# Performance work log

Measured on AMD Instinct MI355X. Metric: run time of the kernel, lower is better.

## Reference

```python
import jax, jax.numpy as jnp
import numpy as np

N = 20000      # nodes
E = 320000     # edges
D = 512        # width
L = 4          # layers
VOCAB = 256
MAX_POS = 256
EPS = 1e-5


def setup_inputs() -> dict:
    key = jax.random.key(0)
    ks = jax.random.split(key, 12)
    tokens = jax.random.randint(ks[0], (N,), 0, VOCAB)
    pos = jax.random.randint(ks[1], (N,), 0, MAX_POS)
    edge_index = jax.random.randint(ks[2], (2, E), 0, N)
    vocab_emb = jax.random.normal(ks[3], (VOCAB, D), jnp.float32) * 0.05
    pos_emb = jax.random.normal(ks[4], (MAX_POS, D), jnp.float32) * 0.05
    bn_gamma = jnp.ones((L, D), jnp.float32)
    bn_beta = jnp.zeros((L, D), jnp.float32)
    bn_mean = jax.random.normal(ks[5], (L, D), jnp.float32) * 0.1
    bn_var = jax.random.uniform(ks[6], (L, D), jnp.float32, 0.5, 1.5)
    W_rel = jax.random.normal(ks[7], (L, D, D), jnp.float32) * (1.0 / np.sqrt(D))
    b_rel = jnp.zeros((L, D), jnp.float32)
    W_root = jax.random.normal(ks[8], (L, D, D), jnp.float32) * (1.0 / np.sqrt(D))
    return {
        "tokens": tokens, "pos": pos, "edge_index": edge_index,
        "vocab_emb": vocab_emb, "pos_emb": pos_emb,
        "bn_gamma": bn_gamma, "bn_beta": bn_beta,
        "bn_mean": bn_mean, "bn_var": bn_var,
        "W_rel": W_rel, "b_rel": b_rel, "W_root": W_root,
    }


def reference(tokens, pos, edge_index, vocab_emb, pos_emb,
              bn_gamma, bn_beta, bn_mean, bn_var, W_rel, b_rel, W_root):
    src, dst = edge_index[0], edge_index[1]
    # in-degree for mean aggregation (clamped to 1 like PyG mean aggr)
    deg = jax.ops.segment_sum(jnp.ones((E,), jnp.float32), dst, num_segments=N)
    deg = jnp.maximum(deg, 1.0)[:, None]                     # [N,1]

    x = vocab_emb[tokens] + pos_emb[pos]                     # [N,D]
    for l in range(L):
        # BatchNorm1d, eval mode with running stats
        inv = bn_gamma[l] * jax.lax.rsqrt(bn_var[l] + EPS)
        x = (x - bn_mean[l]) * inv + bn_beta[l]
        # GraphConv: W_root x_i + W_rel * mean_{j->i} x_j + b
        agg = jax.ops.segment_sum(x[src], dst, num_segments=N) / deg
        x = agg @ W_rel[l].T + b_rel[l] + x @ W_root[l].T
        x = jax.nn.relu(x)
    return x
```

## Files before the change

### kernel.cpp

```cpp
#include <hip/hip_runtime.h>
#include <cstdint>

#define EPS 1e-5f

typedef __attribute__((ext_vector_type(8))) short bf16x8;
typedef __attribute__((ext_vector_type(4))) float f32x4;

__device__ __forceinline__ unsigned short f2bf(float x) {
    uint32_t u = __float_as_uint(x);
    u += 0x7fffu + ((u >> 16) & 1u);
    return (unsigned short)(u >> 16);
}
__device__ __forceinline__ uint32_t pack2(float lo, float hi) {
    return (uint32_t)f2bf(lo) | ((uint32_t)f2bf(hi) << 16);
}
__device__ __forceinline__ float bflo(uint32_t p) { return __uint_as_float(p << 16); }
__device__ __forceinline__ float bfhi(uint32_t p) { return __uint_as_float(p & 0xffff0000u); }

__device__ __forceinline__ void async_ld16(const void* g, const void* l) {
    __builtin_amdgcn_global_load_lds(
        (const __attribute__((address_space(1))) uint32_t*)(uintptr_t)g,
        (__attribute__((address_space(3))) uint32_t*)(uint32_t)(uintptr_t)l,
        16, 0, 0);
}

__global__ __launch_bounds__(256) void zero_kernel(int* __restrict__ p, int n) {
    int i = blockIdx.x * 256 + threadIdx.x;
    if (i < n) p[i] = 0;
}

__global__ __launch_bounds__(256) void count_kernel(const int* __restrict__ ei,
                                                    int* __restrict__ deg, int E) {
    int e = blockIdx.x * 256 + threadIdx.x;
    if (e < E) atomicAdd(&deg[ei[E + e]], 1);
}

__global__ __launch_bounds__(1024) void scan_kernel(const int* __restrict__ deg,
                                                    int* __restrict__ offsets,
                                                    int* __restrict__ cursor,
                                                    float* __restrict__ deginv, int N) {
    __shared__ int part[1024];
    const int t = threadIdx.x;
    const int CH = (N + 1023) >> 10;
    const int base = t * CH;
    int s = 0;
    for (int j = 0; j < CH; ++j) {
        int idx = base + j;
        if (idx < N) s += deg[idx];
    }
    part[t] = s;
    __syncthreads();
    for (int off = 1; off < 1024; off <<= 1) {
        int add = (t >= off) ? part[t - off] : 0;
        __syncthreads();
        part[t] += add;
        __syncthreads();
    }
    int run = (t == 0) ? 0 : part[t - 1];
    for (int j = 0; j < CH; ++j) {
        int idx = base + j;
        if (idx < N) {
            offsets[idx] = run;
            cursor[idx]  = run;
            int dgi = deg[idx];
            deginv[idx] = 1.0f / (float)(dgi > 0 ? dgi : 1);
            run += dgi;
        }
    }
    if (t == 1023) offsets[N] = run;
}

__global__ __launch_bounds__(256) void fill_kernel(const int* __restrict__ ei,
                                                   int* __restrict__ cursor,
                                                   int* __restrict__ csr, int E) {
    int e = blockIdx.x * 256 + threadIdx.x;
    if (e < E) {
        int dd = ei[E + e];
        int slot = atomicAdd(&cursor[dd], 1);
        csr[slot] = ei[e];
    }
}

__global__ __launch_bounds__(256) void embed_bn_kernel(const int* __restrict__ tok,
                                                       const int* __restrict__ pos,
                                                       const float* __restrict__ vemb,
                                                       const float* __restrict__ pemb,
                                                       const float* __restrict__ gamma,
                                                       const float* __restrict__ beta,
                                                       const float* __restrict__ mean,
                                                       const float* __restrict__ var,
                                                       uint32_t* __restrict__ Acat, int N) {
    const int idx = blockIdx.x * 256 + threadIdx.x;
    if (idx >= N * 128) return;
    const int row = idx >> 7;
    const int c = (idx & 127) * 4;
    const int tk = tok[row];
    const int ps = pos[row];
    const float4 a = *(const float4*)&vemb[(size_t)tk * 512 + c];
    const float4 b = *(const float4*)&pemb[(size_t)ps * 512 + c];
    const float4 g = *(const float4*)&gamma[c];
    const float4 be = *(const float4*)&beta[c];
    const float4 mn = *(const float4*)&mean[c];
    const float4 vr = *(const float4*)&var[c];
    const float y0 = (a.x + b.x - mn.x) * (g.x * rsqrtf(vr.x + EPS)) + be.x;
    const float y1 = (a.y + b.y - mn.y) * (g.y * rsqrtf(vr.y + EPS)) + be.y;
    const float y2 = (a.z + b.z - mn.z) * (g.z * rsqrtf(vr.z + EPS)) + be.z;
    const float y3 = (a.w + b.w - mn.w) * (g.w * rsqrtf(vr.w + EPS)) + be.w;
    uint2 o;
    o.x = pack2(y0, y1);
    o.y = pack2(y2, y3);
    *(uint2*)&Acat[(size_t)row * 512 + (c >> 1)] = o;
}

__global__ __launch_bounds__(256) void castW_kernel(const float* __restrict__ Wroot,
                                                    const float* __restrict__ Wrel,
                                                    uint32_t* __restrict__ Wcat) {
    const int p = blockIdx.x * 256 + threadIdx.x;
    const int o  = p >> 9;
    const int dp = p & 511;
    float2 v;
    if (dp < 256) v = *(const float2*)&Wroot[(size_t)o * 512 + dp * 2];
    else          v = *(const float2*)&Wrel[(size_t)o * 512 + (dp - 256) * 2];
    Wcat[(size_t)o * 512 + dp] = pack2(v.x, v.y);
}

__global__ __launch_bounds__(256) void castW4_kernel(const float* __restrict__ Wroot,
                                                     const float* __restrict__ Wrel,
                                                     uint32_t* __restrict__ Wcat4) {
    const int p = blockIdx.x * 256 + threadIdx.x;
    const int l   = p >> 18;
    const int rem = p & 262143;
    const int o   = rem >> 9;
    const int dp  = rem & 511;
    float2 v;
    if (dp < 256) v = *(const float2*)&Wroot[(size_t)l * 262144 + (size_t)o * 512 + dp * 2];
    else          v = *(const float2*)&Wrel[(size_t)l * 262144 + (size_t)o * 512 + (dp - 256) * 2];
    Wcat4[(size_t)l * 262144 + (size_t)o * 512 + dp] = pack2(v.x, v.y);
}

__global__ __launch_bounds__(256) void aggregate_kernel(uint32_t* __restrict__ Acat,
                                                        const int* __restrict__ offsets,
                                                        const int* __restrict__ csr,
                                                        const float* __restrict__ deginv,
                                                        int N) {
    const int node = blockIdx.x * 4 + (threadIdx.x >> 6);
    if (node >= N) return;
    const int lane = threadIdx.x & 63;
    const int col = lane * 4;
    const int beg = offsets[node];
    const int end = offsets[node + 1];
    float s[8] = {0.f, 0.f, 0.f, 0.f, 0.f, 0.f, 0.f, 0.f};
    int e = beg;
    for (; e + 4 <= end; e += 4) {
        const int i0 = csr[e];
        const int i1 = csr[e + 1];
        const int i2 = csr[e + 2];
        const int i3 = csr[e + 3];
        const uint4 p0 = *(const uint4*)&Acat[(size_t)i0 * 512 + col];
        const uint4 p1 = *(const uint4*)&Acat[(size_t)i1 * 512 + col];
        const uint4 p2 = *(const uint4*)&Acat[(size_t)i2 * 512 + col];
        const uint4 p3 = *(const uint4*)&Acat[(size_t)i3 * 512 + col];
        s[0] += bflo(p0.x) + bflo(p1.x) + bflo(p2.x) + bflo(p3.x);
        s[1] += bfhi(p0.x) + bfhi(p1.x) + bfhi(p2.x) + bfhi(p3.x);
        s[2] += bflo(p0.y) + bflo(p1.y) + bflo(p2.y) + bflo(p3.y);
        s[3] += bfhi(p0.y) + bfhi(p1.y) + bfhi(p2.y) + bfhi(p3.y);
        s[4] += bflo(p0.z) + bflo(p1.z) + bflo(p2.z) + bflo(p3.z);
        s[5] += bfhi(p0.z) + bfhi(p1.z) + bfhi(p2.z) + bfhi(p3.z);
        s[6] += bflo(p0.w) + bflo(p1.w) + bflo(p2.w) + bflo(p3.w);
        s[7] += bfhi(p0.w) + bfhi(p1.w) + bfhi(p2.w) + bfhi(p3.w);
    }
    for (; e < end; ++e) {
        const int i0 = csr[e];
        const uint4 p0 = *(const uint4*)&Acat[(size_t)i0 * 512 + col];
        s[0] += bflo(p0.x); s[1] += bfhi(p0.x);
        s[2] += bflo(p0.y); s[3] += bfhi(p0.y);
        s[4] += bflo(p0.z); s[5] += bfhi(p0.z);
        s[6] += bflo(p0.w); s[7] += bfhi(p0.w);
    }
    const float inv = deginv[node];
    uint4 o;
    o.x = pack2(s[0] * inv, s[1] * inv);
    o.y = pack2(s[2] * inv, s[3] * inv);
    o.z = pack2(s[4] * inv, s[5] * inv);
    o.w = pack2(s[6] * inv, s[7] * inv);
    *(uint4*)&Acat[(size_t)node * 512 + 256 + col] = o;
}

__global__ __launch_bounds__(256) void gemm_bt_bias_relu(const unsigned short* __restrict__ A,
                                                         const unsigned short* __restrict__ B,
                                                         const float* __restrict__ bias,
                                                         const float* __restrict__ gamma,
                                                         const float* __restrict__ beta,
                                                         const float* __restrict__ mean,
                                                         const float* __restrict__ var,
                                                         int last,
                                                         float* __restrict__ C,
                                                         unsigned short* __restrict__ Abn,
                                                         int M, int mt, int rpx) {
    __shared__ __align__(16) unsigned short As[2 * 128 * 32];
    __shared__ __align__(16) unsigned short Bs[2 * 128 * 32];

    const int bid = blockIdx.x;
    const int bm  = (bid & 7) * rpx + ((bid >> 3) >> 2);
    const int bn  = (bid >> 3) & 3;
    if (bm >= mt) return;

    const int t    = threadIdx.x;
    const int lane = t & 63;
    const int wave = t >> 6;
    const int wm = (wave >> 1) * 64;
    const int wn = (wave & 1) * 64;

    const int r  = t >> 2;
    const int kc = t & 3;
    int ar0 = bm * 128 + r;      if (ar0 >= M) ar0 = M - 1;
    int ar1 = bm * 128 + r + 64; if (ar1 >= M) ar1 = M - 1;
    const int br0 = bn * 128 + r;
    const int br1 = br0 + 64;

    const unsigned short* ga0 = A + (size_t)ar0 * 1024 + kc * 8;
    const unsigned short* ga1 = A + (size_t)ar1 * 1024 + kc * 8;
    const unsigned short* gb0 = B + (size_t)br0 * 1024 + kc * 8;
    const unsigned short* gb1 = B + (size_t)br1 * 1024 + kc * 8;

    unsigned short* la00 = &As[r * 32 + kc * 8];
    unsigned short* la10 = &As[(r + 64) * 32 + kc * 8];
    unsigned short* la01 = &As[4096 + r * 32 + kc * 8];
    unsigned short* la11 = &As[4096 + (r + 64) * 32 + kc * 8];
    unsigned short* lb00 = &Bs[r * 32 + kc * 8];
    unsigned short* lb10 = &Bs[(r + 64) * 32 + kc * 8];
    unsigned short* lb01 = &Bs[4096 + r * 32 + kc * 8];
    unsigned short* lb11 = &Bs[4096 + (r + 64) * 32 + kc * 8];

    const f32x4 zero = {0.f, 0.f, 0.f, 0.f};
    f32x4 acc[4][4];
#pragma unroll
    for (int i = 0; i < 4; ++i)
#pragma unroll
        for (int j = 0; j < 4; ++j) acc[i][j] = zero;

    const int lm = lane & 15;
    const int q  = lane >> 4;

    for (int k0 = 0; k0 < 1024; k0 += 64) {
        async_ld16(ga0 + k0,      la00);
        async_ld16(ga0 + k0 + 32, la01);
        async_ld16(ga1 + k0,      la10);
        async_ld16(ga1 + k0 + 32, la11);
        async_ld16(gb0 + k0,      lb00);
        async_ld16(gb0 + k0 + 32, lb01);
        async_ld16(gb1 + k0,      lb10);
        async_ld16(gb1 + k0 + 32, lb11);
        __syncthreads();

        bf16x8 afr[4][2], bfr[4][2];
#pragma unroll
        for (int kk = 0; kk < 2; ++kk) {
#pragma unroll
            for (int mt2 = 0; mt2 < 4; ++mt2)
                afr[mt2][kk] = *(const bf16x8*)&As[kk * 4096 + (wm + mt2 * 16 + lm) * 32 + q * 8];
#pragma unroll
            for (int nt = 0; nt < 4; ++nt)
                bfr[nt][kk] = *(const bf16x8*)&Bs[kk * 4096 + (wn + nt * 16 + lm) * 32 + q * 8];
        }
#pragma unroll
        for (int kk = 0; kk < 2; ++kk)
#pragma unroll
            for (int mt2 = 0; mt2 < 4; ++mt2)
#pragma unroll
                for (int nt = 0; nt < 4; ++nt)
                    acc[mt2][nt] = __builtin_amdgcn_mfma_f32_16x16x32_bf16(
                        afr[mt2][kk], bfr[nt][kk], acc[mt2][nt], 0, 0, 0);
        __syncthreads();
    }

#pragma unroll
    for (int nt = 0; nt < 4; ++nt) {
        const int col = bn * 128 + wn + nt * 16 + lm;
        const float bv = bias[col];
        float bn_inv = 0.f, bn_mb = 0.f;
        if (!last) {
            bn_inv = gamma[col] * rsqrtf(var[col] + EPS);
            bn_mb  = mean[col];
        }
        const float bn_beta = last ? 0.f : beta[col];
#pragma unroll
        for (int mt2 = 0; mt2 < 4; ++mt2) {
            const int row0 = bm * 128 + wm + mt2 * 16 + q * 4;
#pragma unroll
            for (int i = 0; i < 4; ++i) {
                const int row = row0 + i;
                if (row < M) {
                    float v = acc[mt2][nt][i] + bv;
                    v = v > 0.f ? v : 0.f;
                    if (last) {
                        C[(size_t)row * 512 + col] = v;
                    } else {
                        const float y = (v - bn_mb) * bn_inv + bn_beta;
                        Abn[(size_t)row * 1024 + col] = f2bf(y);
                    }
                }
            }
        }
    }
}

extern "C" void kernel_launch(void* const* d_in, const int* in_sizes, int n_in,
                              void* d_out, int out_size, void* d_ws, size_t ws_size,
                              hipStream_t stream) {
    const int*   tokens = (const int*)d_in[0];
    const int*   posi   = (const int*)d_in[1];
    const int*   ei     = (const int*)d_in[2];
    const float* vemb   = (const float*)d_in[3];
    const float* pemb   = (const float*)d_in[4];
    const float* gamma  = (const float*)d_in[5];
    const float* beta   = (const float*)d_in[6];
    const float* mean   = (const float*)d_in[7];
    const float* var    = (const float*)d_in[8];
    const float* Wrel   = (const float*)d_in[9];
    const float* brel   = (const float*)d_in[10];
    const float* Wroot  = (const float*)d_in[11];

    const int N = in_sizes[0];
    const int E = in_sizes[2] / 2;
    float* out = (float*)d_out;

    char* w = (char*)d_ws;
    int*      deg     = (int*)(w);
    int*      offsets = (int*)(w + 80000);
    int*      cursor  = (int*)(w + 160016);
    float*    deginv  = (float*)(w + 240032);
    int*      csr     = (int*)(w + 320048);
    uint32_t* Acat    = (uint32_t*)(w + 1600064);
    uint32_t* Wcat    = (uint32_t*)(w + 42560064);

    const int batched = (ws_size >= 46754368ull) ? 1 : 0;

    zero_kernel<<<(N + 255) / 256, 256, 0, stream>>>(deg, N);
    count_kernel<<<(E + 255) / 256, 256, 0, stream>>>(ei, deg, E);
    scan_kernel<<<1, 1024, 0, stream>>>(deg, offsets, cursor, deginv, N);
    fill_kernel<<<(E + 255) / 256, 256, 0, stream>>>(ei, cursor, csr, E);

    embed_bn_kernel<<<(N * 128 + 255) / 256, 256, 0, stream>>>(
        tokens, posi, vemb, pemb, gamma, beta, mean, var, Acat, N);

    if (batched)
        castW4_kernel<<<4096, 256, 0, stream>>>(Wroot, Wrel, Wcat);

    const int mt  = (N + 127) >> 7;
    const int rpx = (mt + 7) >> 3;
    const int gb  = 8 * rpx * 4;

    for (int l = 0; l < 4; ++l) {
        const int last = (l == 3);
        if (!batched)
            castW_kernel<<<1024, 256, 0, stream>>>(Wroot + (size_t)l * 262144,
                                                   Wrel + (size_t)l * 262144, Wcat);
        aggregate_kernel<<<(N + 3) / 4, 256, 0, stream>>>(Acat, offsets, csr, deginv, N);
        const uint32_t* Wl = batched ? (Wcat + (size_t)l * 262144) : Wcat;
        gemm_bt_bias_relu<<<gb, 256, 0, stream>>>(
            (const unsigned short*)Acat, (const unsigned short*)Wl, brel + l * 512,
            gamma + (l + 1) * 512, beta + (l + 1) * 512,
            mean + (l + 1) * 512, var + (l + 1) * 512,
            last, out, (unsigned short*)Acat, N, mt, rpx);
    }
}
```

Measured before the change: 626.0 us.

## Swizzle GEMM LDS layout, halve K-tile, unroll aggregation gather by 8

```diff
diff --git a/kernel.cpp b/kernel.cpp
--- a/kernel.cpp
+++ b/kernel.cpp
@@ -151,6 +151,40 @@
     const int end = offsets[node + 1];
     float s[8] = {0.f, 0.f, 0.f, 0.f, 0.f, 0.f, 0.f, 0.f};
     int e = beg;
+    for (; e + 8 <= end; e += 8) {
+        const int i0 = csr[e];
+        const int i1 = csr[e + 1];
+        const int i2 = csr[e + 2];
+        const int i3 = csr[e + 3];
+        const int i4 = csr[e + 4];
+        const int i5 = csr[e + 5];
+        const int i6 = csr[e + 6];
+        const int i7 = csr[e + 7];
+        const uint4 p0 = *(const uint4*)&Acat[(size_t)i0 * 512 + col];
+        const uint4 p1 = *(const uint4*)&Acat[(size_t)i1 * 512 + col];
+        const uint4 p2 = *(const uint4*)&Acat[(size_t)i2 * 512 + col];
+        const uint4 p3 = *(const uint4*)&Acat[(size_t)i3 * 512 + col];
+        const uint4 p4 = *(const uint4*)&Acat[(size_t)i4 * 512 + col];
+        const uint4 p5 = *(const uint4*)&Acat[(size_t)i5 * 512 + col];
+        const uint4 p6 = *(const uint4*)&Acat[(size_t)i6 * 512 + col];
+        const uint4 p7 = *(const uint4*)&Acat[(size_t)i7 * 512 + col];
+        s[0] += (bflo(p0.x) + bflo(p1.x)) + (bflo(p2.x) + bflo(p3.x))
+              + (bflo(p4.x) + bflo(p5.x)) + (bflo(p6.x) + bflo(p7.x));
+        s[1] += (bfhi(p0.x) + bfhi(p1.x)) + (bfhi(p2.x) + bfhi(p3.x))
+              + (bfhi(p4.x) + bfhi(p5.x)) + (bfhi(p6.x) + bfhi(p7.x));
+        s[2] += (bflo(p0.y) + bflo(p1.y)) + (bflo(p2.y) + bflo(p3.y))
+              + (bflo(p4.y) + bflo(p5.y)) + (bflo(p6.y) + bflo(p7.y));
+        s[3] += (bfhi(p0.y) + bfhi(p1.y)) + (bfhi(p2.y) + bfhi(p3.y))
+              + (bfhi(p4.y) + bfhi(p5.y)) + (bfhi(p6.y) + bfhi(p7.y));
+        s[4] += (bflo(p0.z) + bflo(p1.z)) + (bflo(p2.z) + bflo(p3.z))
+              + (bflo(p4.z) + bflo(p5.z)) + (bflo(p6.z) + bflo(p7.z));
+        s[5] += (bfhi(p0.z) + bfhi(p1.z)) + (bfhi(p2.z) + bfhi(p3.z))
+              + (bfhi(p4.z) + bfhi(p5.z)) + (bfhi(p6.z) + bfhi(p7.z));
+        s[6] += (bflo(p0.w) + bflo(p1.w)) + (bflo(p2.w) + bflo(p3.w))
+              + (bflo(p4.w) + bflo(p5.w)) + (bflo(p6.w) + bflo(p7.w));
+        s[7] += (bfhi(p0.w) + bfhi(p1.w)) + (bfhi(p2.w) + bfhi(p3.w))
+              + (bfhi(p4.w) + bfhi(p5.w)) + (bfhi(p6.w) + bfhi(p7.w));
+    }
     for (; e + 4 <= end; e += 4) {
         const int i0 = csr[e];
         const int i1 = csr[e + 1];
@@ -197,8 +231,8 @@
                                                          float* __restrict__ C,
                                                          unsigned short* __restrict__ Abn,
                                                          int M, int mt, int rpx) {
-    __shared__ __align__(16) unsigned short As[2 * 128 * 32];
-    __shared__ __align__(16) unsigned short Bs[2 * 128 * 32];
+    __shared__ __align__(16) unsigned short As[128 * 32];
+    __shared__ __align__(16) unsigned short Bs[128 * 32];
 
     const int bid = blockIdx.x;
     const int bm  = (bid & 7) * rpx + ((bid >> 3) >> 2);
@@ -213,24 +247,21 @@
 
     const int r  = t >> 2;
     const int kc = t & 3;
+    const int kg = kc ^ ((r >> 1) & 3);
     int ar0 = bm * 128 + r;      if (ar0 >= M) ar0 = M - 1;
     int ar1 = bm * 128 + r + 64; if (ar1 >= M) ar1 = M - 1;
     const int br0 = bn * 128 + r;
     const int br1 = br0 + 64;
 
-    const unsigned short* ga0 = A + (size_t)ar0 * 1024 + kc * 8;
-    const unsigned short* ga1 = A + (size_t)ar1 * 1024 + kc * 8;
-    const unsigned short* gb0 = B + (size_t)br0 * 1024 + kc * 8;
-    const unsigned short* gb1 = B + (size_t)br1 * 1024 + kc * 8;
-
-    unsigned short* la00 = &As[r * 32 + kc * 8];
-    unsigned short* la10 = &As[(r + 64) * 32 + kc * 8];
-    unsigned short* la01 = &As[4096 + r * 32 + kc * 8];
-    unsigned short* la11 = &As[4096 + (r + 64) * 32 + kc * 8];
-    unsigned short* lb00 = &Bs[r * 32 + kc * 8];
-    unsigned short* lb10 = &Bs[(r + 64) * 32 + kc * 8];
-    unsigned short* lb01 = &Bs[4096 + r * 32 + kc * 8];
-    unsigned short* lb11 = &Bs[4096 + (r + 64) * 32 + kc * 8];
+    const unsigned short* ga0 = A + (size_t)ar0 * 1024 + kg * 8;
+    const unsigned short* ga1 = A + (size_t)ar1 * 1024 + kg * 8;
+    const unsigned short* gb0 = B + (size_t)br0 * 1024 + kg * 8;
+    const unsigned short* gb1 = B + (size_t)br1 * 1024 + kg * 8;
+
+    unsigned short* la0 = &As[r * 32 + kc * 8];
+    unsigned short* la1 = &As[(r + 64) * 32 + kc * 8];
+    unsigned short* lb0 = &Bs[r * 32 + kc * 8];
+    unsigned short* lb1 = &Bs[(r + 64) * 32 + kc * 8];
 
     const f32x4 zero = {0.f, 0.f, 0.f, 0.f};
     f32x4 acc[4][4];
@@ -241,36 +272,28 @@
 
     const int lm = lane & 15;
     const int q  = lane >> 4;
-
-    for (int k0 = 0; k0 < 1024; k0 += 64) {
-        async_ld16(ga0 + k0,      la00);
-        async_ld16(ga0 + k0 + 32, la01);
-        async_ld16(ga1 + k0,      la10);
-        async_ld16(ga1 + k0 + 32, la11);
-        async_ld16(gb0 + k0,      lb00);
-        async_ld16(gb0 + k0 + 32, lb01);
-        async_ld16(gb1 + k0,      lb10);
-        async_ld16(gb1 + k0 + 32, lb11);
+    const int qs = (q ^ ((lm >> 1) & 3)) * 8;
+
+    for (int k0 = 0; k0 < 1024; k0 += 32) {
+        async_ld16(ga0 + k0, la0);
+        async_ld16(ga1 + k0, la1);
+        async_ld16(gb0 + k0, lb0);
+        async_ld16(gb1 + k0, lb1);
         __syncthreads();
 
-        bf16x8 afr[4][2], bfr[4][2];
-#pragma unroll
-        for (int kk = 0; kk < 2; ++kk) {
-#pragma unroll
-            for (int mt2 = 0; mt2 < 4; ++mt2)
-                afr[mt2][kk] = *(const bf16x8*)&As[kk * 4096 + (wm + mt2 * 16 + lm) * 32 + q * 8];
+        bf16x8 afr[4], bfr[4];
+#pragma unroll
+        for (int mt2 = 0; mt2 < 4; ++mt2)
+            afr[mt2] = *(const bf16x8*)&As[(wm + mt2 * 16 + lm) * 32 + qs];
+#pragma unroll
+        for (int nt = 0; nt < 4; ++nt)
+            bfr[nt] = *(const bf16x8*)&Bs[(wn + nt * 16 + lm) * 32 + qs];
+#pragma unroll
+        for (int mt2 = 0; mt2 < 4; ++mt2)
 #pragma unroll
             for (int nt = 0; nt < 4; ++nt)
-                bfr[nt][kk] = *(const bf16x8*)&Bs[kk * 4096 + (wn + nt * 16 + lm) * 32 + q * 8];
-        }
-#pragma unroll
-        for (int kk = 0; kk < 2; ++kk)
-#pragma unroll
-            for (int mt2 = 0; mt2 < 4; ++mt2)
-#pragma unroll
-                for (int nt = 0; nt < 4; ++nt)
-                    acc[mt2][nt] = __builtin_amdgcn_mfma_f32_16x16x32_bf16(
-                        afr[mt2][kk], bfr[nt][kk], acc[mt2][nt], 0, 0, 0);
+                acc[mt2][nt] = __builtin_amdgcn_mfma_f32_16x16x32_bf16(afr[mt2], bfr[nt],
+                                                                       acc[mt2][nt], 0, 0, 0);
         __syncthreads();
     }
 
```

Result: faster. 535.8 us (-14.4%).
